# Optimization experiments

Hardware: AMD Instinct MI355X
Metric: run time of the kernel (lower is better)

## Reference

```python
import jax, jax.numpy as jnp
import numpy as np

EPS = 1e-12
K_APPNP = 3
ALPHA = 0.5

def setup_inputs() -> dict:
    key = jax.random.key(0)
    kg, kz, k1, k2, k3 = jax.random.split(key, 5)
    N, out_dim, hid_dim = 10000, 128, 256
    g = jax.random.uniform(kg, (N, N), dtype=jnp.float32)
    z = jax.random.normal(kz, (N, out_dim), dtype=jnp.float32)
    def xavier(k, shape):
        fan_out, fan_in = shape
        lim = float(np.sqrt(6.0 / (fan_in + fan_out)))
        return jax.random.uniform(k, shape, jnp.float32, -lim, lim)
    # torch Linear weight is [out_features, in_features]
    W1 = xavier(k1, (hid_dim, out_dim))    # res1: out_dim -> hid_dim
    W1_ = xavier(k2, (hid_dim, hid_dim))   # res1_: hid -> hid
    W2 = xavier(k3, (out_dim, hid_dim))    # res2: hid -> out_dim
    return {"g": g, "z": z, "W1": W1, "W1_": W1_, "W2": W2}

def _graph_conv(g, x, W, act):
    # dropout is identity in eval mode
    return act((g @ x) @ W.T)

def _appnp(g, H):
    Z = H
    for _ in range(K_APPNP):
        Z = (1.0 - ALPHA) * (g @ Z) + ALPHA * H
    return Z

def reference(g, z, W1, W1_, W2):
    z1 = _graph_conv(g, z, W1, jax.nn.relu)       # [N, hid]
    z_ = _graph_conv(g, z1, W1_, jax.nn.relu)     # [N, hid]
    # torch.tensor(z_) detaches from the autograd graph
    zn = jax.lax.stop_gradient(z_)
    norm = jnp.maximum(jnp.linalg.norm(zn, axis=1, keepdims=True), EPS)
    zn = zn / norm                                 # F.normalize(p=2, dim=1)
    Z = _appnp(g, zn)                              # [N, hid]
    res = _graph_conv(g, z_, W2, jax.nn.sigmoid)   # [N, out]
    return (res, Z)
```

## Files before the change

kernel.cpp:

```cpp
#include <hip/hip_runtime.h>
#include <stdint.h>

typedef __attribute__((ext_vector_type(8))) short short8;
typedef __attribute__((ext_vector_type(4))) float f32x4;
typedef __attribute__((ext_vector_type(4))) unsigned short us4;

#define MFMA16(a,b,c) __builtin_amdgcn_mfma_f32_16x16x32_bf16((a),(b),(c),0,0,0)

static __device__ __forceinline__ float bf2f(unsigned short u){
  union { float f; unsigned int i; } c; c.i = ((unsigned int)u) << 16; return c.f;
}
static __device__ __forceinline__ unsigned short f2bf(float f){
  union { float f; unsigned int i; } c; c.f = f;
  unsigned int x = c.i;
  unsigned int r = x + 0x7fffu + ((x >> 16) & 1u);
  return (unsigned short)(r >> 16);
}
static __device__ __forceinline__ short8 pack8(const float* v){
  short8 r;
  #pragma unroll
  for (int i = 0; i < 8; ++i) r[i] = (short)f2bf(v[i]);
  return r;
}

typedef const __attribute__((address_space(1))) void cg_void;
typedef __attribute__((address_space(3))) void lds_void;
static __device__ __forceinline__ void gl_lds16(const void* g, void* l){
  __builtin_amdgcn_global_load_lds((cg_void*)g, (lds_void*)l, 16, 0, 0);
}

#define MROWS 10240LL
#define LDA   10048
#define GTILE 16384LL

__global__ void k_zero(unsigned short* __restrict__ Tbuf){
  short8 z = {0,0,0,0,0,0,0,0};
  for (int c = blockIdx.x*256 + threadIdx.x; c < 512*6; c += gridDim.x*256){
    int row = c/6, k = c%6;
    *(short8*)(Tbuf + (long long)row*LDA + 10000 + k*8) = z;
  }
}

__global__ void k_conv_w(const float* __restrict__ a, unsigned short* __restrict__ oa, int na4,
                         const float* __restrict__ b, unsigned short* __restrict__ ob, int nb4,
                         const float* __restrict__ c, unsigned short* __restrict__ oc, int nc4){
  for (int i = blockIdx.x*blockDim.x + threadIdx.x; i < na4 + nb4 + nc4;
       i += gridDim.x*blockDim.x){
    const float* src; unsigned short* dst; int j = i;
    if (j < na4){ src = a; dst = oa; }
    else if (j < na4 + nb4){ j -= na4; src = b; dst = ob; }
    else { j -= na4 + nb4; src = c; dst = oc; }
    float4 f = *(const float4*)(src + (long long)j*4);
    us4 v; v.x=f2bf(f.x); v.y=f2bf(f.y); v.z=f2bf(f.z); v.w=f2bf(f.w);
    *(us4*)(dst + (long long)j*4) = v;
  }
}

__global__ void k_tconv_z(const float* __restrict__ z, unsigned short* __restrict__ o){
  __shared__ unsigned short t[64][65];
  const int rb = blockIdx.x*64, cb = blockIdx.y*64;
  #pragma unroll
  for (int it = 0; it < 4; ++it){
    int idx = it*256 + threadIdx.x;
    int r = idx >> 4, c4 = (idx & 15) * 4;
    float4 f = {0.f,0.f,0.f,0.f};
    if (rb + r < 10000) f = *(const float4*)(z + (long long)(rb+r)*128 + cb + c4);
    t[c4+0][r] = f2bf(f.x); t[c4+1][r] = f2bf(f.y);
    t[c4+2][r] = f2bf(f.z); t[c4+3][r] = f2bf(f.w);
  }
  __syncthreads();
  #pragma unroll
  for (int it = 0; it < 4; ++it){
    int idx = it*256 + threadIdx.x;
    int ro = idx >> 4, co4 = (idx & 15) * 4;
    us4 v; v.x=t[ro][co4]; v.y=t[ro][co4+1]; v.z=t[ro][co4+2]; v.w=t[ro][co4+3];
    *(us4*)(o + (long long)(cb+ro)*LDA + rb + co4) = v;
  }
}

__global__ __launch_bounds__(512)
void k_gemm_t0(const float* __restrict__ g, const unsigned short* __restrict__ zT,
               unsigned short* __restrict__ g16, unsigned short* __restrict__ P, int S)
{
  constexpr int ldp = 128;
  __shared__ unsigned short sm[2][24576];

  const int tid = threadIdx.x;
  const int wid = tid >> 6, l = tid & 63;
  const int wm = wid >> 1, wn = wid & 1;
  const int lr = l & 15, lk = l >> 4;
  const int mtile = blockIdx.x;
  const int mBase = mtile * 256;
  const int s = blockIdx.z;
  const int kt0 = (157*s)/S, kt1 = (157*(s+1))/S;

  int arow[4], acol8[4];
  #pragma unroll
  for (int i = 0; i < 4; ++i){
    int ch = tid + 512*i;
    int row = ch >> 3, gr = ch & 7;
    arow[i] = row; acol8[i] = ((gr ^ (row & 7)) * 8);
  }
  float fA[4][8];
  auto loadA = [&](int kt){
    #pragma unroll
    for (int i = 0; i < 4; ++i){
      int grow = mBase + arow[i];
      int col = kt*64 + acol8[i];
      if (grow < 10000 && col < 10000){
        float4 x = *(const float4*)(g + (long long)grow*10000 + col);
        float4 y = *(const float4*)(g + (long long)grow*10000 + col + 4);
        fA[i][0]=x.x; fA[i][1]=x.y; fA[i][2]=x.z; fA[i][3]=x.w;
        fA[i][4]=y.x; fA[i][5]=y.y; fA[i][6]=y.z; fA[i][7]=y.w;
      } else {
        #pragma unroll
        for (int j = 0; j < 8; ++j) fA[i][j] = 0.f;
      }
    }
  };
  auto writeA = [&](int buf, int kt){
    unsigned short* gt = g16 + ((long long)mtile*157 + kt)*GTILE;
    #pragma unroll
    for (int i = 0; i < 4; ++i){
      int ch = tid + 512*i;
      short8 v = pack8(fA[i]);
      *(short8*)(&sm[buf][ch*8]) = v;
      *(short8*)(gt + ch*8) = v;
    }
  };
  auto stageB = [&](int buf, int kt){
    unsigned short* dst = &sm[buf][16384];
    const unsigned short* Bk = zT + (long long)kt*64;
    #pragma unroll
    for (int i = 0; i < 2; ++i){
      int c = i*512 + tid; int row = c >> 3, gr = c & 7;
      gl_lds16(Bk + (long long)row*LDA + ((gr ^ (row & 7))*8), dst + c*8);
    }
  };

  f32x4 acc[4][4];
  #pragma unroll
  for (int i = 0; i < 4; ++i)
    #pragma unroll
    for (int j = 0; j < 4; ++j){ f32x4 zz = {0.f,0.f,0.f,0.f}; acc[i][j] = zz; }

  loadA(kt0); stageB(0, kt0); writeA(0, kt0);
  int cur = 0;
  for (int kt = kt0; kt < kt1; ++kt){
    __syncthreads();
    const bool pf = (kt + 1 < kt1);
    if (pf){ loadA(kt+1); stageB(cur^1, kt+1); }
    const unsigned short* sp = &sm[cur][0];
    #pragma unroll
    for (int ks = 0; ks < 2; ++ks){
      short8 a[4];
      #pragma unroll
      for (int i = 0; i < 4; ++i){
        int row = wm*64 + i*16 + lr;
        a[i] = *(const short8*)(sp + row*64 + (((4*ks+lk) ^ (row & 7))*8));
      }
      #pragma unroll
      for (int j = 0; j < 4; ++j){
        int rb = wn*64 + j*16 + lr;
        short8 b = *(const short8*)(sp + 16384 + rb*64 + (((4*ks+lk) ^ (rb & 7))*8));
        #pragma unroll
        for (int i = 0; i < 4; ++i)
          acc[i][j] = MFMA16(a[i], b, acc[i][j]);
      }
    }
    if (pf) writeA(cur^1, kt+1);
    cur ^= 1;
  }

  unsigned short* Pp = P + (long long)s*MROWS*ldp;
  #pragma unroll
  for (int i = 0; i < 4; ++i){
    const int row0 = mBase + wm*64 + i*16 + lk*4;
    #pragma unroll
    for (int j = 0; j < 4; ++j){
      const int col = wn*64 + j*16 + lr;
      #pragma unroll
      for (int r = 0; r < 4; ++r)
        Pp[(long long)(row0+r)*ldp + col] = f2bf(acc[i][j][r]);
    }
  }
}

template<int BN>
__global__ __launch_bounds__(512)
void k_gemm8(const unsigned short* __restrict__ A,
             const unsigned short* __restrict__ B,
             unsigned short* __restrict__ P, int S, int ldp, int nBase)
{
  constexpr int WNS = BN/4;
  constexpr int NJ  = WNS/16;
  constexpr int BCH = BN/64;
  __shared__ unsigned short sm[2][16384 + BN*64];

  const int tid = threadIdx.x;
  const int wid = tid >> 6, l = tid & 63;
  const int wm = wid >> 2, wn = wid & 3;
  const int lr = l & 15, lk = l >> 4;
  const int mBase = blockIdx.x * 256;
  const int s = blockIdx.z;
  const int kt0 = (157*s)/S, kt1 = (157*(s+1))/S;

  const unsigned short* Abase = A + (long long)blockIdx.x*157*GTILE + tid*8;
  const unsigned short* gsrcB[BCH];
  int ldstB[BCH];
  #pragma unroll
  for (int i = 0; i < BCH; ++i){
    int ch = tid + 512*i;
    int row = ch >> 3, gc = (ch & 7) ^ (row & 7);
    gsrcB[i] = B + (long long)(nBase + row)*LDA + gc*8;
    ldstB[i] = 16384 + ch*8;
  }
  auto stage_tile = [&](unsigned short* dst, int kt){
    const unsigned short* Ak = Abase + (long long)kt*GTILE;
    #pragma unroll
    for (int i = 0; i < 4; ++i)
      gl_lds16(Ak + i*4096, dst + tid*8 + i*4096);
    const long long ko = (long long)kt * 64;
    #pragma unroll
    for (int i = 0; i < BCH; ++i)
      gl_lds16(gsrcB[i] + ko, dst + ldstB[i]);
  };

  f32x4 acc[8][NJ];
  #pragma unroll
  for (int i = 0; i < 8; ++i)
    #pragma unroll
    for (int j = 0; j < NJ; ++j){ f32x4 zz = {0.f,0.f,0.f,0.f}; acc[i][j] = zz; }

  stage_tile(&sm[0][0], kt0);

  int cur = 0;
  for (int kt = kt0; kt < kt1; ++kt){
    const bool pf = (kt + 1 < kt1);
    unsigned short* nb = &sm[cur ^ 1][0];
    const unsigned short* sp = &sm[cur][0];

    if (pf){
      stage_tile(nb, kt + 1);
      __builtin_amdgcn_sched_barrier(0);
      if constexpr (BN == 256) asm volatile("s_waitcnt vmcnt(8)" ::: "memory");
      else                     asm volatile("s_waitcnt vmcnt(6)" ::: "memory");
    } else {
      asm volatile("s_waitcnt vmcnt(0)" ::: "memory");
    }
    __builtin_amdgcn_sched_barrier(0);
    __builtin_amdgcn_s_barrier();
    __builtin_amdgcn_sched_barrier(0);

    short8 bfr[NJ][2];
    #pragma unroll
    for (int jj = 0; jj < NJ; ++jj){
      const int row = wn*WNS + jj*16 + lr;
      #pragma unroll
      for (int ks = 0; ks < 2; ++ks)
        bfr[jj][ks] = *(const short8*)(sp + 16384 + row*64 + (((ks*4+lk) ^ (row & 7))*8));
    }
    #pragma unroll
    for (int ih = 0; ih < 2; ++ih){
      short8 af[4][2];
      #pragma unroll
      for (int ii = 0; ii < 4; ++ii){
        const int row = wm*128 + ih*64 + ii*16 + lr;
        #pragma unroll
        for (int ks = 0; ks < 2; ++ks)
          af[ii][ks] = *(const short8*)(sp + row*64 + (((ks*4+lk) ^ (row & 7))*8));
      }
      __builtin_amdgcn_s_setprio(1);
      #pragma unroll
      for (int ks = 0; ks < 2; ++ks)
        #pragma unroll
        for (int ii = 0; ii < 4; ++ii)
          #pragma unroll
          for (int jj = 0; jj < NJ; ++jj)
            acc[ih*4+ii][jj] = MFMA16(af[ii][ks], bfr[jj][ks], acc[ih*4+ii][jj]);
      __builtin_amdgcn_s_setprio(0);
    }
    __builtin_amdgcn_sched_barrier(0);
    __builtin_amdgcn_s_barrier();
    __builtin_amdgcn_sched_barrier(0);
    cur ^= 1;
  }

  unsigned short* Pp = P + (long long)s*MROWS*ldp;
  #pragma unroll
  for (int i = 0; i < 8; ++i){
    const int row0 = mBase + wm*128 + i*16 + lk*4;
    #pragma unroll
    for (int j = 0; j < NJ; ++j){
      const int col = nBase + wn*WNS + j*16 + lr;
      #pragma unroll
      for (int r = 0; r < 4; ++r)
        Pp[(long long)(row0+r)*ldp + col] = f2bf(acc[i][j][r]);
    }
  }
}

template<int NW, int KW, int LDP, int S, int MODE>
__global__ __launch_bounds__(320)
void k_small(const unsigned short* __restrict__ P,
             const unsigned short* __restrict__ W,
             unsigned short* __restrict__ o1,
             unsigned short* __restrict__ o2,
             unsigned short* __restrict__ o3,
             int doRelu)
{
  const int tid = threadIdx.x, w = tid >> 6, l = tid & 63;
  const int lr = l & 15, lk = l >> 4;
  const int mBase = blockIdx.x * 80;
  constexpr int NF = NW/16;
  constexpr long long SSTR = MROWS*(long long)LDP;

  f32x4 acc[NF];
  #pragma unroll
  for (int f = 0; f < NF; ++f){ f32x4 zz = {0.f,0.f,0.f,0.f}; acc[f] = zz; }

  const unsigned short* ap = P + (long long)(mBase + 16*w + lr)*LDP + lk*8;
  #pragma unroll
  for (int kc = 0; kc < KW/32; ++kc){
    float av[8];
    short8 v0 = *(const short8*)(ap + kc*32);
    #pragma unroll
    for (int e = 0; e < 8; ++e) av[e] = bf2f((unsigned short)v0[e]);
    #pragma unroll
    for (int s2 = 1; s2 < S; ++s2){
      short8 v = *(const short8*)(ap + (long long)s2*SSTR + kc*32);
      #pragma unroll
      for (int e = 0; e < 8; ++e) av[e] += bf2f((unsigned short)v[e]);
    }
    short8 a = pack8(av);
    #pragma unroll
    for (int f = 0; f < NF; ++f){
      short8 b = *(const short8*)(W + (long long)(16*f+lr)*KW + kc*32 + lk*8);
      acc[f] = MFMA16(a, b, acc[f]);
    }
  }

  const int row0 = mBase + 16*w + lk*4;
  if constexpr (MODE == 0){
    #pragma unroll
    for (int f = 0; f < NF; ++f){
      us4 v;
      #pragma unroll
      for (int r = 0; r < 4; ++r){
        float x = acc[f][r];
        if (doRelu) x = fmaxf(x, 0.0f);
        v[r] = f2bf(x);
      }
      *(us4*)(o1 + (long long)(16*f+lr)*LDA + row0) = v;
    }
  } else {
    float ss[4] = {0.f,0.f,0.f,0.f};
    #pragma unroll
    for (int f = 0; f < NF; ++f)
      #pragma unroll
      for (int r = 0; r < 4; ++r){
        float v = fmaxf(acc[f][r], 0.0f);
        acc[f][r] = v;
        ss[r] += v*v;
      }
    #pragma unroll
    for (int r = 0; r < 4; ++r){
      #pragma unroll
      for (int off = 1; off <= 8; off <<= 1)
        ss[r] += __shfl_xor(ss[r], off, 64);
      ss[r] = 1.0f / fmaxf(sqrtf(ss[r]), 1e-12f);
    }
    #pragma unroll
    for (int f = 0; f < NF; ++f){
      const int col = 16*f + lr;
      us4 vn;
      #pragma unroll
      for (int r = 0; r < 4; ++r){
        float zr = acc[f][r];
        float nr = zr * ss[r];
        vn[r] = f2bf(nr);
        o2[(long long)(row0+r)*256 + col] = vn[r];
        o3[(long long)(row0+r)*256 + col] = f2bf(zr);
      }
      *(us4*)(o1 + (long long)col*LDA + row0) = vn;
    }
  }
}

__global__ void k_reduce_T(const unsigned short* __restrict__ P, int S, int ldp, int colOff,
                           unsigned short* __restrict__ outT,
                           const unsigned short* __restrict__ H)
{
  __shared__ unsigned short t[64][65];
  const int rb = blockIdx.x*64, cb = blockIdx.y*64;
  const long long stride = MROWS * (long long)ldp;
  #pragma unroll
  for (int it = 0; it < 4; ++it){
    int idx = it*256 + threadIdx.x;
    int r = idx >> 4, c4 = (idx & 15)*4;
    int row = rb + r;
    float sv[4] = {0.f,0.f,0.f,0.f};
    if (row < 10000){
      const unsigned short* p = P + (long long)row*ldp + colOff + cb + c4;
      for (int s2 = 0; s2 < S; ++s2){
        us4 tt = *(const us4*)(p + (long long)s2*stride);
        sv[0] += bf2f(tt.x); sv[1] += bf2f(tt.y);
        sv[2] += bf2f(tt.z); sv[3] += bf2f(tt.w);
      }
      us4 h = *(const us4*)(H + (long long)row*256 + cb + c4);
      sv[0] = 0.5f*sv[0] + 0.5f*bf2f(h.x);
      sv[1] = 0.5f*sv[1] + 0.5f*bf2f(h.y);
      sv[2] = 0.5f*sv[2] + 0.5f*bf2f(h.z);
      sv[3] = 0.5f*sv[3] + 0.5f*bf2f(h.w);
    }
    t[c4+0][r] = f2bf(sv[0]); t[c4+1][r] = f2bf(sv[1]);
    t[c4+2][r] = f2bf(sv[2]); t[c4+3][r] = f2bf(sv[3]);
  }
  __syncthreads();
  #pragma unroll
  for (int it = 0; it < 4; ++it){
    int idx = it*256 + threadIdx.x;
    int ro = idx >> 4, co4 = (idx & 15)*4;
    us4 v; v.x=t[ro][co4]; v.y=t[ro][co4+1]; v.z=t[ro][co4+2]; v.w=t[ro][co4+3];
    *(us4*)(outT + (long long)(cb+ro)*LDA + rb + co4) = v;
  }
}

__global__ void k_reduce_sig(const unsigned short* __restrict__ P, int S,
                             float* __restrict__ out)
{
  const long long stride = MROWS * 128LL;
  const int idx = blockIdx.x*256 + threadIdx.x;
  const int row = idx >> 5;
  const int c4 = (idx & 31)*4;
  const unsigned short* p = P + (long long)row*128 + c4;
  float sv[4] = {0.f,0.f,0.f,0.f};
  for (int s2 = 0; s2 < S; ++s2){
    us4 tt = *(const us4*)(p + (long long)s2*stride);
    sv[0] += bf2f(tt.x); sv[1] += bf2f(tt.y);
    sv[2] += bf2f(tt.z); sv[3] += bf2f(tt.w);
  }
  float4 o;
  o.x = 1.0f/(1.0f + expf(-sv[0]));
  o.y = 1.0f/(1.0f + expf(-sv[1]));
  o.z = 1.0f/(1.0f + expf(-sv[2]));
  o.w = 1.0f/(1.0f + expf(-sv[3]));
  *(float4*)(out + (long long)row*128 + c4) = o;
}

__global__ void k_reduce2(const unsigned short* __restrict__ P, int S, int ldp,
                          float* __restrict__ out, const unsigned short* __restrict__ H)
{
  const long long stride = MROWS * (long long)ldp;
  const int idx = blockIdx.x*256 + threadIdx.x;
  const int row = idx >> 6;
  const int c4 = (idx & 63)*4;
  const unsigned short* p = P + (long long)row*ldp + c4;
  float sv[4] = {0.f,0.f,0.f,0.f};
  for (int s2 = 0; s2 < S; ++s2){
    us4 tt = *(const us4*)(p + (long long)s2*stride);
    sv[0] += bf2f(tt.x); sv[1] += bf2f(tt.y);
    sv[2] += bf2f(tt.z); sv[3] += bf2f(tt.w);
  }
  us4 h = *(const us4*)(H + (long long)row*256 + c4);
  float4 o;
  o.x = 0.5f*sv[0] + 0.5f*bf2f(h.x);
  o.y = 0.5f*sv[1] + 0.5f*bf2f(h.y);
  o.z = 0.5f*sv[2] + 0.5f*bf2f(h.z);
  o.w = 0.5f*sv[3] + 0.5f*bf2f(h.w);
  *(float4*)(out + (long long)row*256 + c4) = o;
}

extern "C" void kernel_launch(void* const* d_in, const int* in_sizes, int n_in,
                              void* d_out, int out_size, void* d_ws, size_t ws_size,
                              hipStream_t stream)
{
  const float* g   = (const float*)d_in[0];
  const float* z   = (const float*)d_in[1];
  const float* W1  = (const float*)d_in[2];
  const float* W1_ = (const float*)d_in[3];
  const float* W2  = (const float*)d_in[4];

  char* ws = (char*)d_ws;
  size_t off = 0;
  auto alloc = [&](size_t bytes)->void*{
    void* p = ws + off; off += (bytes + 255) & ~(size_t)255; return p;
  };
  unsigned short* g16  = (unsigned short*)alloc(40ULL*157*GTILE*2);
  unsigned short* zT   = (unsigned short*)alloc(128ULL*10048*2);
  unsigned short* W1c  = (unsigned short*)alloc(256ULL*128*2);
  unsigned short* W1_c = (unsigned short*)alloc(256ULL*256*2);
  unsigned short* W2c  = (unsigned short*)alloc(128ULL*256*2);
  unsigned short* Tbuf = (unsigned short*)alloc(512ULL*10048*2);
  unsigned short* zn   = (unsigned short*)alloc(10000ULL*256*2);
  unsigned short* Xbuf = (unsigned short*)alloc(10000ULL*256*2);
  unsigned short* P    = (unsigned short*)alloc(10240ULL*1536*2);
  (void)ws_size; (void)in_sizes; (void)n_in; (void)out_size;

  float* res  = (float*)d_out;
  float* Zout = (float*)d_out + 10000LL*128;
  unsigned short* y2T = Tbuf + 256LL*LDA;

  k_zero<<<dim3(12), dim3(256), 0, stream>>>(Tbuf);
  k_tconv_z<<<dim3(157,2), dim3(256), 0, stream>>>(z, zT);
  k_conv_w<<<dim3(120), dim3(256), 0, stream>>>(W1, W1c, 256*128/4,
                                                W1_, W1_c, 256*256/4,
                                                W2, W2c, 128*256/4);

  k_gemm_t0<<<dim3(40,1,6), dim3(512), 0, stream>>>(g, zT, g16, P, 6);
  k_small<256,128,128,6,0><<<dim3(125), dim3(320), 0, stream>>>(P, W1c, Tbuf, nullptr, nullptr, 1);
  k_gemm8<256><<<dim3(40,1,6), dim3(512), 0, stream>>>(g16, Tbuf, P, 6, 256, 0);
  k_small<256,256,256,6,1><<<dim3(125), dim3(320), 0, stream>>>(P, W1_c, Tbuf, zn, Xbuf, 0);
  k_small<128,256,256,1,0><<<dim3(125), dim3(320), 0, stream>>>(Xbuf, W2c, y2T, nullptr, nullptr, 0);
  k_gemm8<256><<<dim3(40,1,6), dim3(512), 0, stream>>>(g16, Tbuf, P, 6, 256, 0);
  k_reduce_T<<<dim3(157,4), dim3(256), 0, stream>>>(P, 6, 256, 0, Tbuf, zn);
  k_gemm8<128><<<dim3(40,1,6), dim3(512), 0, stream>>>(g16, y2T, P, 6, 128, 0);
  k_reduce_sig<<<dim3(1250), dim3(256), 0, stream>>>(P, 6, res);
  k_gemm8<256><<<dim3(40,1,6), dim3(512), 0, stream>>>(g16, Tbuf, P, 6, 256, 0);
  k_reduce_T<<<dim3(157,4), dim3(256), 0, stream>>>(P, 6, 256, 0, Tbuf, zn);
  k_gemm8<256><<<dim3(40,1,6), dim3(512), 0, stream>>>(g16, Tbuf, P, 6, 256, 0);
  k_reduce2<<<dim3(2500), dim3(256), 0, stream>>>(P, 6, 256, Zout, zn);
}
```

Measured before the change: 542.9 us.

## Load B operand fragments directly from global memory instead of staging through LDS

Both the first-layer GEMM and the main graph GEMM stop staging the B (transposed feature) tile through shared memory. Each wave now loads its MFMA B fragments straight from global memory into registers every k-step. This cuts LDS footprint and LDS traffic, and it also drops the hand-tuned vmcnt waits, split barriers and setprio scheduling in favour of a plain __syncthreads. The cost is that global-load latency for B now sits directly in the critical path of each iteration without prefetch, and different waves re-read the same B data through cache.

```diff
diff --git a/kernel.cpp b/kernel.cpp
--- a/kernel.cpp
+++ b/kernel.cpp
@@ -83,7 +83,7 @@
                unsigned short* __restrict__ g16, unsigned short* __restrict__ P, int S)
 {
   constexpr int ldp = 128;
-  __shared__ unsigned short sm[2][24576];
+  __shared__ unsigned short sm[2][16384];
 
   const int tid = threadIdx.x;
   const int wid = tid >> 6, l = tid & 63;
@@ -128,15 +128,11 @@
       *(short8*)(gt + ch*8) = v;
     }
   };
-  auto stageB = [&](int buf, int kt){
-    unsigned short* dst = &sm[buf][16384];
-    const unsigned short* Bk = zT + (long long)kt*64;
-    #pragma unroll
-    for (int i = 0; i < 2; ++i){
-      int c = i*512 + tid; int row = c >> 3, gr = c & 7;
-      gl_lds16(Bk + (long long)row*LDA + ((gr ^ (row & 7))*8), dst + c*8);
-    }
-  };
+
+  const unsigned short* Brow[4];
+  #pragma unroll
+  for (int j = 0; j < 4; ++j)
+    Brow[j] = zT + (long long)(wn*64 + j*16 + lr)*LDA + lk*8;
 
   f32x4 acc[4][4];
   #pragma unroll
@@ -144,12 +140,18 @@
     #pragma unroll
     for (int j = 0; j < 4; ++j){ f32x4 zz = {0.f,0.f,0.f,0.f}; acc[i][j] = zz; }
 
-  loadA(kt0); stageB(0, kt0); writeA(0, kt0);
+  loadA(kt0); writeA(0, kt0);
   int cur = 0;
   for (int kt = kt0; kt < kt1; ++kt){
     __syncthreads();
+    short8 bfr[4][2];
+    #pragma unroll
+    for (int j = 0; j < 4; ++j)
+      #pragma unroll
+      for (int ks = 0; ks < 2; ++ks)
+        bfr[j][ks] = *(const short8*)(Brow[j] + (long long)kt*64 + ks*32);
     const bool pf = (kt + 1 < kt1);
-    if (pf){ loadA(kt+1); stageB(cur^1, kt+1); }
+    if (pf) loadA(kt+1);
     const unsigned short* sp = &sm[cur][0];
     #pragma unroll
     for (int ks = 0; ks < 2; ++ks){
@@ -160,13 +162,10 @@
         a[i] = *(const short8*)(sp + row*64 + (((4*ks+lk) ^ (row & 7))*8));
       }
       #pragma unroll
-      for (int j = 0; j < 4; ++j){
-        int rb = wn*64 + j*16 + lr;
-        short8 b = *(const short8*)(sp + 16384 + rb*64 + (((4*ks+lk) ^ (rb & 7))*8));
+      for (int j = 0; j < 4; ++j)
         #pragma unroll
         for (int i = 0; i < 4; ++i)
-          acc[i][j] = MFMA16(a[i], b, acc[i][j]);
-      }
+          acc[i][j] = MFMA16(a[i], bfr[j][ks], acc[i][j]);
     }
     if (pf) writeA(cur^1, kt+1);
     cur ^= 1;
@@ -188,14 +187,13 @@
 
 template<int BN>
 __global__ __launch_bounds__(512)
-void k_gemm8(const unsigned short* __restrict__ A,
+void k_gemmD(const unsigned short* __restrict__ A,
              const unsigned short* __restrict__ B,
              unsigned short* __restrict__ P, int S, int ldp, int nBase)
 {
   constexpr int WNS = BN/4;
   constexpr int NJ  = WNS/16;
-  constexpr int BCH = BN/64;
-  __shared__ unsigned short sm[2][16384 + BN*64];
+  __shared__ unsigned short sm[2][16384];
 
   const int tid = threadIdx.x;
   const int wid = tid >> 6, l = tid & 63;
@@ -206,60 +204,39 @@
   const int kt0 = (157*s)/S, kt1 = (157*(s+1))/S;
 
   const unsigned short* Abase = A + (long long)blockIdx.x*157*GTILE + tid*8;
-  const unsigned short* gsrcB[BCH];
-  int ldstB[BCH];
-  #pragma unroll
-  for (int i = 0; i < BCH; ++i){
-    int ch = tid + 512*i;
-    int row = ch >> 3, gc = (ch & 7) ^ (row & 7);
-    gsrcB[i] = B + (long long)(nBase + row)*LDA + gc*8;
-    ldstB[i] = 16384 + ch*8;
-  }
-  auto stage_tile = [&](unsigned short* dst, int kt){
+  auto stageA = [&](unsigned short* dst, int kt){
     const unsigned short* Ak = Abase + (long long)kt*GTILE;
     #pragma unroll
     for (int i = 0; i < 4; ++i)
       gl_lds16(Ak + i*4096, dst + tid*8 + i*4096);
-    const long long ko = (long long)kt * 64;
-    #pragma unroll
-    for (int i = 0; i < BCH; ++i)
-      gl_lds16(gsrcB[i] + ko, dst + ldstB[i]);
   };
 
+  const unsigned short* Brow[NJ];
+  #pragma unroll
+  for (int jj = 0; jj < NJ; ++jj)
+    Brow[jj] = B + (long long)(nBase + wn*WNS + jj*16 + lr)*LDA + lk*8;
+
   f32x4 acc[8][NJ];
   #pragma unroll
   for (int i = 0; i < 8; ++i)
     #pragma unroll
     for (int j = 0; j < NJ; ++j){ f32x4 zz = {0.f,0.f,0.f,0.f}; acc[i][j] = zz; }
 
-  stage_tile(&sm[0][0], kt0);
+  stageA(&sm[0][0], kt0);
 
   int cur = 0;
   for (int kt = kt0; kt < kt1; ++kt){
+    __syncthreads();
+    short8 bfr[NJ][2];
+    #pragma unroll
+    for (int jj = 0; jj < NJ; ++jj)
+      #pragma unroll
+      for (int ks = 0; ks < 2; ++ks)
+        bfr[jj][ks] = *(const short8*)(Brow[jj] + (long long)kt*64 + ks*32);
     const bool pf = (kt + 1 < kt1);
-    unsigned short* nb = &sm[cur ^ 1][0];
+    if (pf) stageA(&sm[cur^1][0], kt+1);
+
     const unsigned short* sp = &sm[cur][0];
-
-    if (pf){
-      stage_tile(nb, kt + 1);
-      __builtin_amdgcn_sched_barrier(0);
-      if constexpr (BN == 256) asm volatile("s_waitcnt vmcnt(8)" ::: "memory");
-      else                     asm volatile("s_waitcnt vmcnt(6)" ::: "memory");
-    } else {
-      asm volatile("s_waitcnt vmcnt(0)" ::: "memory");
-    }
-    __builtin_amdgcn_sched_barrier(0);
-    __builtin_amdgcn_s_barrier();
-    __builtin_amdgcn_sched_barrier(0);
-
-    short8 bfr[NJ][2];
-    #pragma unroll
-    for (int jj = 0; jj < NJ; ++jj){
-      const int row = wn*WNS + jj*16 + lr;
-      #pragma unroll
-      for (int ks = 0; ks < 2; ++ks)
-        bfr[jj][ks] = *(const short8*)(sp + 16384 + row*64 + (((ks*4+lk) ^ (row & 7))*8));
-    }
     #pragma unroll
     for (int ih = 0; ih < 2; ++ih){
       short8 af[4][2];
@@ -270,7 +247,6 @@
         for (int ks = 0; ks < 2; ++ks)
           af[ii][ks] = *(const short8*)(sp + row*64 + (((ks*4+lk) ^ (row & 7))*8));
       }
-      __builtin_amdgcn_s_setprio(1);
       #pragma unroll
       for (int ks = 0; ks < 2; ++ks)
         #pragma unroll
@@ -278,11 +254,7 @@
           #pragma unroll
           for (int jj = 0; jj < NJ; ++jj)
             acc[ih*4+ii][jj] = MFMA16(af[ii][ks], bfr[jj][ks], acc[ih*4+ii][jj]);
-      __builtin_amdgcn_s_setprio(0);
-    }
-    __builtin_amdgcn_sched_barrier(0);
-    __builtin_amdgcn_s_barrier();
-    __builtin_amdgcn_sched_barrier(0);
+    }
     cur ^= 1;
   }
 
@@ -509,15 +481,15 @@
 
   k_gemm_t0<<<dim3(40,1,6), dim3(512), 0, stream>>>(g, zT, g16, P, 6);
   k_small<256,128,128,6,0><<<dim3(125), dim3(320), 0, stream>>>(P, W1c, Tbuf, nullptr, nullptr, 1);
-  k_gemm8<256><<<dim3(40,1,6), dim3(512), 0, stream>>>(g16, Tbuf, P, 6, 256, 0);
+  k_gemmD<256><<<dim3(40,1,6), dim3(512), 0, stream>>>(g16, Tbuf, P, 6, 256, 0);
   k_small<256,256,256,6,1><<<dim3(125), dim3(320), 0, stream>>>(P, W1_c, Tbuf, zn, Xbuf, 0);
   k_small<128,256,256,1,0><<<dim3(125), dim3(320), 0, stream>>>(Xbuf, W2c, y2T, nullptr, nullptr, 0);
-  k_gemm8<256><<<dim3(40,1,6), dim3(512), 0, stream>>>(g16, Tbuf, P, 6, 256, 0);
+  k_gemmD<256><<<dim3(40,1,6), dim3(512), 0, stream>>>(g16, Tbuf, P, 6, 256, 0);
   k_reduce_T<<<dim3(157,4), dim3(256), 0, stream>>>(P, 6, 256, 0, Tbuf, zn);
-  k_gemm8<128><<<dim3(40,1,6), dim3(512), 0, stream>>>(g16, y2T, P, 6, 128, 0);
+  k_gemmD<128><<<dim3(40,1,6), dim3(512), 0, stream>>>(g16, y2T, P, 6, 128, 0);
   k_reduce_sig<<<dim3(1250), dim3(256), 0, stream>>>(P, 6, res);
-  k_gemm8<256><<<dim3(40,1,6), dim3(512), 0, stream>>>(g16, Tbuf, P, 6, 256, 0);
+  k_gemmD<256><<<dim3(40,1,6), dim3(512), 0, stream>>>(g16, Tbuf, P, 6, 256, 0);
   k_reduce_T<<<dim3(157,4), dim3(256), 0, stream>>>(P, 6, 256, 0, Tbuf, zn);
-  k_gemm8<256><<<dim3(40,1,6), dim3(512), 0, stream>>>(g16, Tbuf, P, 6, 256, 0);
+  k_gemmD<256><<<dim3(40,1,6), dim3(512), 0, stream>>>(g16, Tbuf, P, 6, 256, 0);
   k_reduce2<<<dim3(2500), dim3(256), 0, stream>>>(P, 6, 256, Zout, zn);
 }
```

Measured after the change: 726.6 us. 33.8% more time.
